# Kernel optimization log

Hardware: AMD Instinct MI355X
Metric: run time of the kernel (lower is better)

Reference implementation:

```python
import jax, jax.numpy as jnp
import numpy as np
from jax import lax

VOCAB, EMBED, HIDDEN = 50000, 300, 512
BATCH, SEQ = 64, 512


def setup_inputs() -> dict:
    key = jax.random.key(0)
    ks = jax.random.split(key, 8)
    return {
        "x_indx": jax.random.randint(ks[0], (BATCH, SEQ), 0, VOCAB),
        "embeddings": jax.random.normal(ks[1], (VOCAB, EMBED), dtype=jnp.float32),
        "W_ih": jax.random.normal(ks[2], (4 * HIDDEN, EMBED), dtype=jnp.float32) * 0.02,
        "W_hh": jax.random.normal(ks[3], (4 * HIDDEN, HIDDEN), dtype=jnp.float32) * 0.02,
        "b_ih": jax.random.normal(ks[4], (4 * HIDDEN,), dtype=jnp.float32) * 0.02,
        "b_hh": jax.random.normal(ks[5], (4 * HIDDEN,), dtype=jnp.float32) * 0.02,
        "W_out": jax.random.normal(ks[6], (1, HIDDEN), dtype=jnp.float32) * 0.02,
        "b_out": jax.random.normal(ks[7], (1,), dtype=jnp.float32) * 0.02,
    }


def _lstm_final_hidden(x, W_ih, W_hh, b_ih, b_hh):
    # x: [B, S, E] -> final hidden state h_T: [B, H]
    B = x.shape[0]
    H = W_hh.shape[1]
    # Precompute input projections for all timesteps: [S, B, 4H]
    x_proj = jnp.einsum('bse,ge->sbg', x, W_ih) + b_ih + b_hh

    def step(carry, xp):
        h, c = carry
        gates = xp + h @ W_hh.T  # [B, 4H], PyTorch gate order i,f,g,o
        i, f, g, o = jnp.split(gates, 4, axis=-1)
        i = jax.nn.sigmoid(i)
        f = jax.nn.sigmoid(f)
        g = jnp.tanh(g)
        o = jax.nn.sigmoid(o)
        c = f * c + i * g
        h = o * jnp.tanh(c)
        return (h, c), None

    h0 = jnp.zeros((B, H), dtype=x.dtype)
    c0 = jnp.zeros((B, H), dtype=x.dtype)
    (hT, cT), _ = lax.scan(step, (h0, c0), x_proj)
    return hT


def reference(x_indx, embeddings, W_ih, W_hh, b_ih, b_hh, W_out, b_out):
    # Frozen embedding lookup: [B, S, E]
    x = embeddings[x_indx]
    hT = _lstm_final_hidden(x, W_ih, W_hh, b_ih, b_hh)  # [B, H]
    return hT @ W_out.T + b_out  # [B, 1]
```

## Files before the change

### kernel.cpp

```cpp
#include <hip/hip_runtime.h>
#include <hip/hip_bf16.h>

typedef short  bf16x8 __attribute__((ext_vector_type(8)));
typedef float  f32x4  __attribute__((ext_vector_type(4)));
typedef int    i32x4  __attribute__((ext_vector_type(4)));

#define BB 64
#define SS 512
#define EE 300
#define HH 512

#define XT_OFF     ((size_t)0)
#define XT_BYTES   ((size_t)SS*10*4*1024)
#define SLOT_OFF   (XT_OFF + XT_BYTES)
#define SLOT_BYTES ((size_t)2*64*2*64*16)
#define HT_OFF     (SLOT_OFF + SLOT_BYTES)
#define HT_BYTES   ((size_t)BB*HH*4)

__device__ __forceinline__ unsigned short f2bf(float x) {
  union { float f; unsigned u; } v; v.f = x;
  unsigned r = v.u + 0x7fffu + ((v.u >> 16) & 1u);
  return (unsigned short)(r >> 16);
}
__device__ __forceinline__ float sigm(float x) { return 1.f / (1.f + __expf(-x)); }
__device__ __forceinline__ float tanh_fast(float x) { return 1.f - 2.f / (__expf(2.f * x) + 1.f); }

__device__ __forceinline__ void ld16_cc(i32x4* dst, const void* p) {
  asm volatile("global_load_dwordx4 %0, %1, off sc0 sc1"
               : "=v"(*dst) : "v"(p) : "memory");
}
__device__ __forceinline__ void st16_cc(void* p, i32x4 v) {
  asm volatile("global_store_dwordx4 %0, %1, off sc0 sc1"
               :: "v"(p), "v"(v) : "memory");
}

__global__ void gather_cast_kernel(const int* __restrict__ idx,
                                   const float* __restrict__ emb,
                                   unsigned short* __restrict__ xt) {
  __shared__ unsigned short lds_x[16 * 320];
  const int t     = blockIdx.x >> 2;
  const int mtile = blockIdx.x & 3;
  const int tid   = threadIdx.x;

  const int c2 = tid >> 4;
  const int e0 = tid & 15;
  const int b  = mtile * 16 + c2;
  const int vocab = idx[b * SS + t];
  const float* src = emb + (size_t)vocab * EE;
  for (int e = e0; e < 320; e += 16)
    lds_x[c2 * 320 + e] = (e < EE) ? f2bf(src[e]) : (unsigned short)0;
  __syncthreads();

  unsigned short* outb = xt + (((size_t)t * 10) * 4 + mtile) * 512;
  #pragma unroll
  for (int rr = 0; rr < 3; ++rr) {
    int O = rr * 4096 + tid * 16;
    if (O < 10240) {
      int ks = O >> 10;
      int inblk = O & 1023;
      int c  = inblk >> 6;
      int kg = (inblk >> 4) & 3;
      bf16x8 v = *(const bf16x8*)&lds_x[c * 320 + ks * 32 + kg * 8];
      *(bf16x8*)((char*)outb + (size_t)ks * 4096 + inblk) = v;
    }
  }
}

__launch_bounds__(512)
__global__ void lstm_kernel(const unsigned short* __restrict__ xt,
                            char* __restrict__ slots,
                            float* __restrict__ hT,
                            const float* __restrict__ Wih,
                            const float* __restrict__ Whh,
                            const float* __restrict__ bih,
                            const float* __restrict__ bhh) {
  __shared__ float glds[2][2][64][33];

  const int p    = blockIdx.x;
  const int tid  = threadIdx.x;
  const int l    = tid & 63;
  const int w    = tid >> 6;
  const int mt   = w & 3;
  const int kh   = w >> 2;
  const int c    = l & 15;
  const int kg   = l >> 4;

  bf16x8 Bx[2][5], Bh[2][8];
  #pragma unroll
  for (int T = 0; T < 2; ++T) {
    const int Grow = ((c >> 2) << 9) + (p << 3) + (T << 2) + (c & 3);
    const float* wih_row = Wih + (size_t)Grow * EE;
    const float* whh_row = Whh + (size_t)Grow * HH;
    #pragma unroll
    for (int ks = 0; ks < 5; ++ks) {
      int k0 = 32 * (5 * kh + ks) + 8 * kg;
      bf16x8 vb;
      #pragma unroll
      for (int j = 0; j < 8; ++j) {
        int k = k0 + j;
        vb[j] = (short)((k < EE) ? f2bf(wih_row[k]) : (unsigned short)0);
      }
      Bx[T][ks] = vb;
    }
    #pragma unroll
    for (int ks = 0; ks < 8; ++ks) {
      int k0 = 32 * (8 * kh + ks) + 8 * kg;
      bf16x8 vb;
      #pragma unroll
      for (int j = 0; j < 8; ++j) vb[j] = (short)f2bf(whh_row[k0 + j]);
      Bh[T][ks] = vb;
    }
  }

  const int u     = l & 7;
  const int sl    = l >> 3;
  const int sglob = 16 * mt + 8 * kh + sl;
  const float bi  = bih[(p << 3) + u]        + bhh[(p << 3) + u];
  const float bf_ = bih[512  + (p << 3) + u] + bhh[512  + (p << 3) + u];
  const float bg  = bih[1024 + (p << 3) + u] + bhh[1024 + (p << 3) + u];
  const float bo  = bih[1536 + (p << 3) + u] + bhh[1536 + (p << 3) + u];
  float cstate = 0.f;

  const unsigned short* xbase = xt + ((size_t)(5 * kh) * 4 + mt) * 512
                                   + (c << 5) + (kg << 3);
  const int rd_in = ((32 * kh + kg) << 11) + ((16 * mt + c) << 4);
  char* const wr_base = slots + ((size_t)p << 11) + (((size_t)(u >> 2)) << 10)
                              + ((size_t)sglob << 4);
  const int colp = ((c >> 2) << 3) + (c & 3);

  for (int it = 0; it < SS; ++it) {
    f32x4 acc0 = {0.f, 0.f, 0.f, 0.f};
    f32x4 acc1 = {0.f, 0.f, 0.f, 0.f};

    const unsigned short* xp = xbase + (size_t)it * 20480;
    #pragma unroll
    for (int ks = 0; ks < 5; ++ks) {
      bf16x8 a = *(const bf16x8*)(xp + (size_t)ks * 2048);
      acc0 = __builtin_amdgcn_mfma_f32_16x16x32_bf16(a, Bx[0][ks], acc0, 0, 0, 0);
      acc1 = __builtin_amdgcn_mfma_f32_16x16x32_bf16(a, Bx[1][ks], acc1, 0, 0, 0);
    }

    const char* rp = slots + (size_t)(it & 1) * 131072 + rd_in;
    i32x4 sl_[8][2];
    for (;;) {
      #pragma unroll
      for (int ks = 0; ks < 8; ++ks) {
        ld16_cc(&sl_[ks][0], rp + ks * 8192);
        ld16_cc(&sl_[ks][1], rp + ks * 8192 + 1024);
      }
      asm volatile("s_waitcnt vmcnt(0)" ::: "memory");
      __builtin_amdgcn_sched_barrier(0);
      int ok = 1;
      #pragma unroll
      for (int ks = 0; ks < 8; ++ks)
        ok &= (sl_[ks][0][2] == it) & (sl_[ks][1][2] == it);
      if (__all(ok)) break;
      __builtin_amdgcn_s_sleep(1);
    }
    #pragma unroll
    for (int ks = 0; ks < 8; ++ks) {
      i32x4 t;
      t[0] = sl_[ks][0][0]; t[1] = sl_[ks][0][1];
      t[2] = sl_[ks][1][0]; t[3] = sl_[ks][1][1];
      bf16x8 a = __builtin_bit_cast(bf16x8, t);
      acc0 = __builtin_amdgcn_mfma_f32_16x16x32_bf16(a, Bh[0][ks], acc0, 0, 0, 0);
      acc1 = __builtin_amdgcn_mfma_f32_16x16x32_bf16(a, Bh[1][ks], acc1, 0, 0, 0);
    }

    #pragma unroll
    for (int r = 0; r < 4; ++r) {
      glds[it & 1][kh][16 * mt + 4 * kg + r][colp]     = acc0[r];
      glds[it & 1][kh][16 * mt + 4 * kg + r][colp + 4] = acc1[r];
    }
    __syncthreads();

    const float* g0 = &glds[it & 1][0][sglob][0];
    const float* g1 = &glds[it & 1][1][sglob][0];
    float gi = g0[u]      + g1[u]      + bi;
    float gf = g0[u + 8]  + g1[u + 8]  + bf_;
    float gg = g0[u + 16] + g1[u + 16] + bg;
    float go = g0[u + 24] + g1[u + 24] + bo;
    float ig = sigm(gi);
    float fg = sigm(gf);
    float gt = tanh_fast(gg);
    float og = sigm(go);
    cstate = fg * cstate + ig * gt;
    float h = og * tanh_fast(cstate);

    if (it != SS - 1) {
      int hv  = (int)f2bf(h);
      int o1  = __shfl_xor(hv, 1, 64);
      int pk  = (hv & 0xffff) | (o1 << 16);
      int pk2 = __shfl_xor(pk, 2, 64);
      if ((u & 3) == 0) {
        i32x4 val; val[0] = pk; val[1] = pk2; val[2] = it + 1; val[3] = 0;
        st16_cc(wr_base + (size_t)((it + 1) & 1) * 131072, val);
      }
    } else {
      hT[(size_t)sglob * HH + (p << 3) + u] = h;
    }
  }
}

__global__ void outproj_kernel(const float* __restrict__ hT,
                               const float* __restrict__ Wout,
                               const float* __restrict__ bout,
                               float* __restrict__ y) {
  int b = blockIdx.x;
  int t = threadIdx.x;
  float s = 0.f;
  for (int j = t; j < HH; j += 64) s += hT[b * HH + j] * Wout[j];
  #pragma unroll
  for (int off = 32; off > 0; off >>= 1) s += __shfl_down(s, off, 64);
  if (t == 0) y[b] = s + bout[0];
}

extern "C" void kernel_launch(void* const* d_in, const int* in_sizes, int n_in,
                              void* d_out, int out_size, void* d_ws, size_t ws_size,
                              hipStream_t stream) {
  const int*   idx  = (const int*)d_in[0];
  const float* emb  = (const float*)d_in[1];
  const float* Wih  = (const float*)d_in[2];
  const float* Whh  = (const float*)d_in[3];
  const float* bih  = (const float*)d_in[4];
  const float* bhh  = (const float*)d_in[5];
  const float* Wout = (const float*)d_in[6];
  const float* bout = (const float*)d_in[7];
  float* y = (float*)d_out;

  char* ws = (char*)d_ws;
  unsigned short* xt = (unsigned short*)(ws + XT_OFF);
  char* slots        = ws + SLOT_OFF;
  float* hT          = (float*)(ws + HT_OFF);

  hipMemsetAsync(slots, 0, SLOT_BYTES, stream);

  gather_cast_kernel<<<SS * 4, 256, 0, stream>>>(idx, emb, xt);
  lstm_kernel<<<64, 512, 0, stream>>>(xt, slots, hT, Wih, Whh, bih, bhh);
  outproj_kernel<<<BB, 64, 0, stream>>>(hT, Wout, bout, y);
}
```

Before: 1.941 ms.

## Split LSTM recurrence by batch group so each block syncs only within its group

The recurrent kernel is restructured so each of the 64 blocks owns one 16-row batch group and 32 hidden units. Each wave covers the full K range for 4 units, which removes the cross-wave K-split reduction through LDS. Hidden-state exchange now goes through per-batch-group slots, so a block waits only on the 16 blocks sharing its group rather than all 64. Each lane polls four 16-byte slots and stages them in LDS for the MFMA A operand. This adds LDS staging and a barrier per step, and raises register pressure because each lane holds 26 weight fragments, while launch bounds now request two blocks per CU.

```diff
diff --git a/kernel.cpp b/kernel.cpp
--- a/kernel.cpp
+++ b/kernel.cpp
@@ -13,7 +13,7 @@
 #define XT_OFF     ((size_t)0)
 #define XT_BYTES   ((size_t)SS*10*4*1024)
 #define SLOT_OFF   (XT_OFF + XT_BYTES)
-#define SLOT_BYTES ((size_t)2*64*2*64*16)
+#define SLOT_BYTES ((size_t)2*4*16*128*16)
 #define HT_OFF     (SLOT_OFF + SLOT_BYTES)
 #define HT_BYTES   ((size_t)BB*HH*4)
 
@@ -66,7 +66,7 @@
   }
 }
 
-__launch_bounds__(512)
+__launch_bounds__(512, 2)
 __global__ void lstm_kernel(const unsigned short* __restrict__ xt,
                             char* __restrict__ slots,
                             float* __restrict__ hT,
@@ -74,130 +74,131 @@
                             const float* __restrict__ Whh,
                             const float* __restrict__ bih,
                             const float* __restrict__ bhh) {
-  __shared__ float glds[2][2][64][33];
-
-  const int p    = blockIdx.x;
-  const int tid  = threadIdx.x;
-  const int l    = tid & 63;
-  const int w    = tid >> 6;
-  const int mt   = w & 3;
-  const int kh   = w >> 2;
-  const int c    = l & 15;
-  const int kg   = l >> 4;
-
-  bf16x8 Bx[2][5], Bh[2][8];
-  #pragma unroll
-  for (int T = 0; T < 2; ++T) {
-    const int Grow = ((c >> 2) << 9) + (p << 3) + (T << 2) + (c & 3);
-    const float* wih_row = Wih + (size_t)Grow * EE;
-    const float* whh_row = Whh + (size_t)Grow * HH;
-    #pragma unroll
-    for (int ks = 0; ks < 5; ++ks) {
-      int k0 = 32 * (5 * kh + ks) + 8 * kg;
-      bf16x8 vb;
-      #pragma unroll
-      for (int j = 0; j < 8; ++j) {
-        int k = k0 + j;
-        vb[j] = (short)((k < EE) ? f2bf(wih_row[k]) : (unsigned short)0);
+  __shared__ __attribute__((aligned(16))) char hstage[2][16 * 1280];
+
+  const int p   = blockIdx.x;
+  const int sg  = p & 3;
+  const int uw  = p >> 2;
+  const int tid = threadIdx.x;
+  const int l   = tid & 63;
+  const int w   = tid >> 6;
+  const int c   = l & 15;
+  const int kg  = l >> 4;
+  const int U0  = 32 * uw + 4 * w;
+
+  const int Grow = ((c >> 2) << 9) + U0 + (c & 3);
+  const float* wih_row = Wih + (size_t)Grow * EE;
+  const float* whh_row = Whh + (size_t)Grow * HH;
+
+  bf16x8 Bx[10], Bh[16];
+  #pragma unroll
+  for (int ks = 0; ks < 10; ++ks) {
+    int k0 = 32 * ks + 8 * kg;
+    bf16x8 vb;
+    #pragma unroll
+    for (int j = 0; j < 8; ++j) {
+      int k = k0 + j;
+      vb[j] = (short)((k < EE) ? f2bf(wih_row[k]) : (unsigned short)0);
+    }
+    Bx[ks] = vb;
+  }
+  #pragma unroll
+  for (int kt = 0; kt < 16; ++kt) {
+    int k0 = 32 * kt + 8 * kg;
+    bf16x8 vb;
+    #pragma unroll
+    for (int j = 0; j < 8; ++j) vb[j] = (short)f2bf(whh_row[k0 + j]);
+    Bh[kt] = vb;
+  }
+  const float bsum = bih[Grow] + bhh[Grow];
+
+  const unsigned short* xbase = xt + sg * 512 + c * 32 + kg * 8;
+
+  const int uq_t = tid & 127;
+  const int s0_t = tid >> 7;
+  const int lwb  = (uq_t >> 3) * 1280 + ((uq_t >> 1) & 3) * 16 + (uq_t & 1) * 8
+                 + s0_t * 80;
+  const size_t sg_off = (size_t)sg * 32768;
+  const char* rbase = slots + sg_off + (size_t)tid * 16;
+  const int lr = c * 80 + kg * 16;
+  char* const wbase = slots + sg_off + (size_t)(8 * uw + w) * 16;
+
+  f32x4 cst = {0.f, 0.f, 0.f, 0.f};
+
+  for (int it = 0; it < SS; ++it) {
+    const char* rp = rbase + (size_t)(it & 1) * 131072;
+    i32x4 d0, d1, d2, d3;
+    ld16_cc(&d0, rp);
+    ld16_cc(&d1, rp + 8192);
+    ld16_cc(&d2, rp + 16384);
+    ld16_cc(&d3, rp + 24576);
+
+    f32x4 ax0 = {0.f, 0.f, 0.f, 0.f};
+    f32x4 ax1 = {0.f, 0.f, 0.f, 0.f};
+    const unsigned short* xq = xbase + (size_t)it * 20480;
+    #pragma unroll
+    for (int ks = 0; ks < 10; ks += 2) {
+      bf16x8 a0 = *(const bf16x8*)(xq + ks * 2048);
+      bf16x8 a1 = *(const bf16x8*)(xq + (ks + 1) * 2048);
+      ax0 = __builtin_amdgcn_mfma_f32_16x16x32_bf16(a0, Bx[ks],     ax0, 0, 0, 0);
+      ax1 = __builtin_amdgcn_mfma_f32_16x16x32_bf16(a1, Bx[ks + 1], ax1, 0, 0, 0);
+    }
+    __builtin_amdgcn_sched_barrier(0);
+
+    asm volatile("s_waitcnt vmcnt(0)" ::: "memory");
+    while (!((d0[2] == it) & (d1[2] == it) & (d2[2] == it) & (d3[2] == it))) {
+      __builtin_amdgcn_s_sleep(1);
+      ld16_cc(&d0, rp);
+      ld16_cc(&d1, rp + 8192);
+      ld16_cc(&d2, rp + 16384);
+      ld16_cc(&d3, rp + 24576);
+      asm volatile("s_waitcnt vmcnt(0)" ::: "memory");
+    }
+
+    char* hs = hstage[it & 1];
+    { int* q = (int*)(hs + lwb);        q[0] = d0[0]; q[1] = d0[1]; }
+    { int* q = (int*)(hs + lwb + 320);  q[0] = d1[0]; q[1] = d1[1]; }
+    { int* q = (int*)(hs + lwb + 640);  q[0] = d2[0]; q[1] = d2[1]; }
+    { int* q = (int*)(hs + lwb + 960);  q[0] = d3[0]; q[1] = d3[1]; }
+    __syncthreads();
+
+    f32x4 ah0 = {0.f, 0.f, 0.f, 0.f};
+    f32x4 ah1 = {0.f, 0.f, 0.f, 0.f};
+    #pragma unroll
+    for (int kt = 0; kt < 16; kt += 2) {
+      bf16x8 a0 = *(const bf16x8*)(hs + kt * 1280 + lr);
+      bf16x8 a1 = *(const bf16x8*)(hs + (kt + 1) * 1280 + lr);
+      ah0 = __builtin_amdgcn_mfma_f32_16x16x32_bf16(a0, Bh[kt],     ah0, 0, 0, 0);
+      ah1 = __builtin_amdgcn_mfma_f32_16x16x32_bf16(a1, Bh[kt + 1], ah1, 0, 0, 0);
+    }
+    f32x4 acc = (ax0 + ax1) + (ah0 + ah1);
+
+    char* wp = wbase + (size_t)((it + 1) & 1) * 131072;
+    #pragma unroll
+    for (int r = 0; r < 4; ++r) {
+      float v  = acc[r] + bsum;
+      float vf = __shfl_xor(v, 4, 64);
+      float vg = __shfl_xor(v, 8, 64);
+      float vo = __shfl_xor(v, 12, 64);
+      float ig = sigm(v);
+      float fg = sigm(vf);
+      float gt = tanh_fast(vg);
+      float og = sigm(vo);
+      cst[r] = fg * cst[r] + ig * gt;
+      float h = og * tanh_fast(cst[r]);
+
+      if (it != SS - 1) {
+        int hv  = (int)f2bf(h);
+        int o1  = __shfl_xor(hv, 1, 64);
+        int pk  = (hv & 0xffff) | (o1 << 16);
+        int pk2 = __shfl_xor(pk, 2, 64);
+        if (c == 0) {
+          i32x4 val; val[0] = pk; val[1] = pk2; val[2] = it + 1; val[3] = 0;
+          st16_cc(wp + (4 * kg + r) * 2048, val);
+        }
+      } else if (c < 4) {
+        hT[(size_t)(16 * sg + 4 * kg + r) * HH + U0 + c] = h;
       }
-      Bx[T][ks] = vb;
-    }
-    #pragma unroll
-    for (int ks = 0; ks < 8; ++ks) {
-      int k0 = 32 * (8 * kh + ks) + 8 * kg;
-      bf16x8 vb;
-      #pragma unroll
-      for (int j = 0; j < 8; ++j) vb[j] = (short)f2bf(whh_row[k0 + j]);
-      Bh[T][ks] = vb;
-    }
-  }
-
-  const int u     = l & 7;
-  const int sl    = l >> 3;
-  const int sglob = 16 * mt + 8 * kh + sl;
-  const float bi  = bih[(p << 3) + u]        + bhh[(p << 3) + u];
-  const float bf_ = bih[512  + (p << 3) + u] + bhh[512  + (p << 3) + u];
-  const float bg  = bih[1024 + (p << 3) + u] + bhh[1024 + (p << 3) + u];
-  const float bo  = bih[1536 + (p << 3) + u] + bhh[1536 + (p << 3) + u];
-  float cstate = 0.f;
-
-  const unsigned short* xbase = xt + ((size_t)(5 * kh) * 4 + mt) * 512
-                                   + (c << 5) + (kg << 3);
-  const int rd_in = ((32 * kh + kg) << 11) + ((16 * mt + c) << 4);
-  char* const wr_base = slots + ((size_t)p << 11) + (((size_t)(u >> 2)) << 10)
-                              + ((size_t)sglob << 4);
-  const int colp = ((c >> 2) << 3) + (c & 3);
-
-  for (int it = 0; it < SS; ++it) {
-    f32x4 acc0 = {0.f, 0.f, 0.f, 0.f};
-    f32x4 acc1 = {0.f, 0.f, 0.f, 0.f};
-
-    const unsigned short* xp = xbase + (size_t)it * 20480;
-    #pragma unroll
-    for (int ks = 0; ks < 5; ++ks) {
-      bf16x8 a = *(const bf16x8*)(xp + (size_t)ks * 2048);
-      acc0 = __builtin_amdgcn_mfma_f32_16x16x32_bf16(a, Bx[0][ks], acc0, 0, 0, 0);
-      acc1 = __builtin_amdgcn_mfma_f32_16x16x32_bf16(a, Bx[1][ks], acc1, 0, 0, 0);
-    }
-
-    const char* rp = slots + (size_t)(it & 1) * 131072 + rd_in;
-    i32x4 sl_[8][2];
-    for (;;) {
-      #pragma unroll
-      for (int ks = 0; ks < 8; ++ks) {
-        ld16_cc(&sl_[ks][0], rp + ks * 8192);
-        ld16_cc(&sl_[ks][1], rp + ks * 8192 + 1024);
-      }
-      asm volatile("s_waitcnt vmcnt(0)" ::: "memory");
-      __builtin_amdgcn_sched_barrier(0);
-      int ok = 1;
-      #pragma unroll
-      for (int ks = 0; ks < 8; ++ks)
-        ok &= (sl_[ks][0][2] == it) & (sl_[ks][1][2] == it);
-      if (__all(ok)) break;
-      __builtin_amdgcn_s_sleep(1);
-    }
-    #pragma unroll
-    for (int ks = 0; ks < 8; ++ks) {
-      i32x4 t;
-      t[0] = sl_[ks][0][0]; t[1] = sl_[ks][0][1];
-      t[2] = sl_[ks][1][0]; t[3] = sl_[ks][1][1];
-      bf16x8 a = __builtin_bit_cast(bf16x8, t);
-      acc0 = __builtin_amdgcn_mfma_f32_16x16x32_bf16(a, Bh[0][ks], acc0, 0, 0, 0);
-      acc1 = __builtin_amdgcn_mfma_f32_16x16x32_bf16(a, Bh[1][ks], acc1, 0, 0, 0);
-    }
-
-    #pragma unroll
-    for (int r = 0; r < 4; ++r) {
-      glds[it & 1][kh][16 * mt + 4 * kg + r][colp]     = acc0[r];
-      glds[it & 1][kh][16 * mt + 4 * kg + r][colp + 4] = acc1[r];
-    }
-    __syncthreads();
-
-    const float* g0 = &glds[it & 1][0][sglob][0];
-    const float* g1 = &glds[it & 1][1][sglob][0];
-    float gi = g0[u]      + g1[u]      + bi;
-    float gf = g0[u + 8]  + g1[u + 8]  + bf_;
-    float gg = g0[u + 16] + g1[u + 16] + bg;
-    float go = g0[u + 24] + g1[u + 24] + bo;
-    float ig = sigm(gi);
-    float fg = sigm(gf);
-    float gt = tanh_fast(gg);
-    float og = sigm(go);
-    cstate = fg * cstate + ig * gt;
-    float h = og * tanh_fast(cstate);
-
-    if (it != SS - 1) {
-      int hv  = (int)f2bf(h);
-      int o1  = __shfl_xor(hv, 1, 64);
-      int pk  = (hv & 0xffff) | (o1 << 16);
-      int pk2 = __shfl_xor(pk, 2, 64);
-      if ((u & 3) == 0) {
-        i32x4 val; val[0] = pk; val[1] = pk2; val[2] = it + 1; val[3] = 0;
-        st16_cc(wr_base + (size_t)((it + 1) & 1) * 131072, val);
-      }
-    } else {
-      hT[(size_t)sglob * HH + (p << 3) + u] = h;
     }
   }
 }
```

Measured after the change: 2.420 ms. 24.7% more time.
